# Kernel optimization log

Hardware: AMD Instinct MI355X
Metric: run time of the kernel (lower is better)

Reference implementation:

```python
import jax, jax.numpy as jnp
import numpy as np

N_NODES = 20000
N_EDGES = 320000
N_GRAPHS = 200
MAX_NODES = 100


def gcn_conv(x, W, b, src, dst, n_nodes):
    # PyG GCNConv: linear transform, add self-loops, symmetric normalization
    h = x @ W                                   # [N, out]
    loop = jnp.arange(n_nodes)
    s = jnp.concatenate([src, loop])
    d = jnp.concatenate([dst, loop])
    deg = jax.ops.segment_sum(jnp.ones_like(s, dtype=h.dtype), d, num_segments=n_nodes)
    dinv = jax.lax.rsqrt(jnp.maximum(deg, 1.0))  # deg >= 1 due to self-loops
    norm = dinv[s] * dinv[d]                     # [E+N]
    msg = h[s] * norm[:, None]                   # gather + scale
    return jax.ops.segment_sum(msg, d, num_segments=n_nodes) + b


def setup_inputs() -> dict:
    key = jax.random.key(0)
    ks = jax.random.split(key, 16)
    IN, H, L = 128, 256, 64
    P = MAX_NODES * (MAX_NODES - 1) // 2
    inp = {
        "x": jax.random.normal(ks[0], (N_NODES, IN), jnp.float32),
        "edge_index": jax.random.randint(ks[1], (2, N_EDGES), 0, N_NODES),
        "batch": jnp.sort(jax.random.randint(ks[2], (N_NODES,), 0, N_GRAPHS)),
        "eps": jax.random.normal(ks[3], (N_GRAPHS, L), jnp.float32),
        "W1": jax.random.normal(ks[4], (IN, H), jnp.float32) * (1.0 / np.sqrt(IN)),
        "b1": jnp.zeros((H,), jnp.float32),
        "W2": jax.random.normal(ks[5], (H, H), jnp.float32) * (1.0 / np.sqrt(H)),
        "b2": jnp.zeros((H,), jnp.float32),
        "Wmu": jax.random.normal(ks[6], (H, L), jnp.float32) * (1.0 / np.sqrt(H)),
        "bmu": jnp.zeros((L,), jnp.float32),
        "Wlv": jax.random.normal(ks[7], (H, L), jnp.float32) * (1.0 / np.sqrt(H)),
        "blv": jnp.zeros((L,), jnp.float32),
        "D1": jax.random.normal(ks[8], (L, H), jnp.float32) * (1.0 / np.sqrt(L)),
        "db1": jnp.zeros((H,), jnp.float32),
        "D2": jax.random.normal(ks[9], (H, H), jnp.float32) * (1.0 / np.sqrt(H)),
        "db2": jnp.zeros((H,), jnp.float32),
        "D3": jax.random.normal(ks[10], (H, P), jnp.float32) * (1.0 / np.sqrt(H)),
        "db3": jnp.zeros((P,), jnp.float32),
    }
    return inp


def reference(x, edge_index, batch, eps, W1, b1, W2, b2, Wmu, bmu, Wlv, blv,
              D1, db1, D2, db2, D3, db3):
    src, dst = edge_index[0], edge_index[1]
    # encoder
    h = jax.nn.relu(gcn_conv(x, W1, b1, src, dst, N_NODES))
    h = jax.nn.relu(gcn_conv(h, W2, b2, src, dst, N_NODES))
    # global mean pool
    sums = jax.ops.segment_sum(h, batch, num_segments=N_GRAPHS)
    cnt = jax.ops.segment_sum(jnp.ones((N_NODES,), h.dtype), batch, num_segments=N_GRAPHS)
    hg = sums / jnp.maximum(cnt, 1.0)[:, None]   # [B, H]
    mu = hg @ Wmu + bmu
    logvar = hg @ Wlv + blv
    # reparameterise
    z = mu + eps * jnp.exp(0.5 * logvar)
    # decoder MLP
    d = jax.nn.relu(z @ D1 + db1)
    d = jax.nn.relu(d @ D2 + db2)
    probs = jax.nn.sigmoid(d @ D3 + db3)         # [B, MAX_NODES*(MAX_NODES-1)//2]
    iu, ju = jnp.triu_indices(MAX_NODES, k=1)
    B = z.shape[0]
    adj = jnp.zeros((B, MAX_NODES, MAX_NODES), probs.dtype)
    adj = adj.at[:, iu, ju].set(probs)
    adj = adj + jnp.swapaxes(adj, 1, 2)
    return adj, mu, logvar
```

## Files before the change

### kernel.cpp

```cpp
#include <hip/hip_runtime.h>
#include <math.h>

#define N_NODES  20000
#define N_EDGES  320000
#define N_GRAPHS 200
#define MAXN     100
#define F_IN     128
#define F_H      256
#define F_L      64
#define P_PAIRS  4950
#define P_PAD    4992
#define ADJ_SIZE (N_GRAPHS * MAXN * MAXN)
#define MU_OFF   ADJ_SIZE
#define LV_OFF   (ADJ_SIZE + N_GRAPHS * F_L)

#define ELL_W    64
#define EF_NB    ((N_EDGES + 255) / 256)

static inline int ceil_div(int a, int b) { return (a + b - 1) / b; }

typedef __attribute__((ext_vector_type(8))) short bf16x8;
typedef __attribute__((ext_vector_type(4))) float f32x4;

static __device__ inline unsigned short f2bf(float f) {
    union { float f; unsigned u; } v; v.f = f;
    unsigned r = (v.u + 0x7FFFu + ((v.u >> 16) & 1u)) >> 16;
    return (unsigned short)r;
}
static __device__ inline float bf2f(unsigned short s) {
    union { unsigned u; float f; } v; v.u = (unsigned)s << 16; return v.f;
}
static __device__ inline float4 ubf4(ushort4 u) {
    float4 f;
    f.x = bf2f(u.x); f.y = bf2f(u.y); f.z = bf2f(u.z); f.w = bf2f(u.w);
    return f;
}
static __device__ inline float rdeg(int d) { return rsqrtf((float)d + 1.0f); }

#define PP_S1  32768
#define PP_S2  98304
#define PP_END 1376256
#define PP_NB  (PP_END / 256)
#define CV_END 640000
#define CV_NB  (CV_END / 256)
__global__ __launch_bounds__(256) void k_prep(
        const int* __restrict__ src, const int* __restrict__ dst,
        int* __restrict__ fill, int* __restrict__ ell,
        const float* __restrict__ W1, const float* __restrict__ W2,
        const float* __restrict__ D3,
        unsigned short* __restrict__ W1p, unsigned short* __restrict__ W2p,
        unsigned short* __restrict__ D3p,
        const float* __restrict__ x, unsigned short* __restrict__ xs) {
    if (blockIdx.x < EF_NB) {
        int e = blockIdx.x * 256 + threadIdx.x;
        if (e < N_EDGES) {
            int d = dst[e];
            int pos = atomicAdd(fill + d, 1);
            if (pos < ELL_W) ell[d * ELL_W + pos] = src[e];
        }
        return;
    }
    if (blockIdx.x < EF_NB + PP_NB) {
        int pid = (blockIdx.x - EF_NB) * 256 + threadIdx.x;
        const float* W; unsigned short* Bp; int N, NP, t;
        if (pid < PP_S1)      { t = pid;          W = W1; Bp = W1p; N = 256;     NP = 256; }
        else if (pid < PP_S2) { t = pid - PP_S1;  W = W2; Bp = W2p; N = 256;     NP = 256; }
        else                  { t = pid - PP_S2;  W = D3; Bp = D3p; N = P_PAIRS; NP = P_PAD; }
        int j    = t & 7;
        int lane = (t >> 3) & 63;
        int tile = t >> 9;
        int NT = NP >> 4;
        int nt = tile % NT;
        int kt = tile / NT;
        int k = kt * 32 + (lane >> 4) * 8 + j;
        int n = nt * 16 + (lane & 15);
        Bp[t] = (n < N) ? f2bf(W[(size_t)k * N + n]) : (unsigned short)0;
        return;
    }
    int tid = (blockIdx.x - EF_NB - PP_NB) * 256 + threadIdx.x;
    if (tid >= CV_END) return;
    float4 val = ((const float4*)x)[tid];
    ushort4 o;
    o.x = f2bf(val.x); o.y = f2bf(val.y);
    o.z = f2bf(val.z); o.w = f2bf(val.w);
    ((ushort4*)xs)[tid] = o;
}

__global__ __launch_bounds__(512) void k_layer1(const unsigned short* __restrict__ xs,
                                                const int* __restrict__ fill,
                                                const int* __restrict__ ell,
                                                const unsigned short* __restrict__ W1p,
                                                const float* __restrict__ bias,
                                                unsigned short* __restrict__ h1s, int M) {
    __shared__ unsigned short At[32 * 128];
    char* Ab = (char*)At;
    const int tid  = threadIdx.x;
    const int lane = tid & 63;
    const int w    = tid >> 6;

    for (int s = 0; s < 4; ++s) {
        int slot = w * 4 + s;
        int v = blockIdx.x * 32 + slot;
        ushort2 ob; ob.x = 0; ob.y = 0;
        if (v < M) {
            int dg  = fill[v];
            int beg = v * ELL_W;
            int end = beg + min(dg, ELL_W);
            float dv = rdeg(dg);
            float2 a0 = make_float2(0.f, 0.f), a1 = make_float2(0.f, 0.f);
            int i = beg;
            for (; i + 8 <= end; i += 8) {
                int s0 = ell[i + 0], s1 = ell[i + 1], s2 = ell[i + 2], s3 = ell[i + 3];
                int s4 = ell[i + 4], s5 = ell[i + 5], s6 = ell[i + 6], s7 = ell[i + 7];
                float r0 = rdeg(fill[s0]), r1 = rdeg(fill[s1]);
                float r2 = rdeg(fill[s2]), r3 = rdeg(fill[s3]);
                float r4 = rdeg(fill[s4]), r5 = rdeg(fill[s5]);
                float r6 = rdeg(fill[s6]), r7 = rdeg(fill[s7]);
                ushort2 u0 = ((const ushort2*)(xs + (size_t)s0 * F_IN))[lane];
                ushort2 u1 = ((const ushort2*)(xs + (size_t)s1 * F_IN))[lane];
                ushort2 u2 = ((const ushort2*)(xs + (size_t)s2 * F_IN))[lane];
                ushort2 u3 = ((const ushort2*)(xs + (size_t)s3 * F_IN))[lane];
                ushort2 u4 = ((const ushort2*)(xs + (size_t)s4 * F_IN))[lane];
                ushort2 u5 = ((const ushort2*)(xs + (size_t)s5 * F_IN))[lane];
                ushort2 u6 = ((const ushort2*)(xs + (size_t)s6 * F_IN))[lane];
                ushort2 u7 = ((const ushort2*)(xs + (size_t)s7 * F_IN))[lane];
                a0.x += r0 * bf2f(u0.x) + r2 * bf2f(u2.x) + r4 * bf2f(u4.x) + r6 * bf2f(u6.x);
                a0.y += r0 * bf2f(u0.y) + r2 * bf2f(u2.y) + r4 * bf2f(u4.y) + r6 * bf2f(u6.y);
                a1.x += r1 * bf2f(u1.x) + r3 * bf2f(u3.x) + r5 * bf2f(u5.x) + r7 * bf2f(u7.x);
                a1.y += r1 * bf2f(u1.y) + r3 * bf2f(u3.y) + r5 * bf2f(u5.y) + r7 * bf2f(u7.y);
            }
            for (; i + 4 <= end; i += 4) {
                int s0 = ell[i + 0], s1 = ell[i + 1], s2 = ell[i + 2], s3 = ell[i + 3];
                float r0 = rdeg(fill[s0]), r1 = rdeg(fill[s1]);
                float r2 = rdeg(fill[s2]), r3 = rdeg(fill[s3]);
                ushort2 u0 = ((const ushort2*)(xs + (size_t)s0 * F_IN))[lane];
                ushort2 u1 = ((const ushort2*)(xs + (size_t)s1 * F_IN))[lane];
                ushort2 u2 = ((const ushort2*)(xs + (size_t)s2 * F_IN))[lane];
                ushort2 u3 = ((const ushort2*)(xs + (size_t)s3 * F_IN))[lane];
                a0.x += r0 * bf2f(u0.x) + r2 * bf2f(u2.x);
                a0.y += r0 * bf2f(u0.y) + r2 * bf2f(u2.y);
                a1.x += r1 * bf2f(u1.x) + r3 * bf2f(u3.x);
                a1.y += r1 * bf2f(u1.y) + r3 * bf2f(u3.y);
            }
            for (; i < end; ++i) {
                int sv = ell[i];
                float rr = rdeg(fill[sv]);
                ushort2 u = ((const ushort2*)(xs + (size_t)sv * F_IN))[lane];
                a0.x += rr * bf2f(u.x); a0.y += rr * bf2f(u.y);
            }
            ushort2 uv = ((const ushort2*)(xs + (size_t)v * F_IN))[lane];
            ob.x = f2bf(dv * (a0.x + a1.x + dv * bf2f(uv.x)));
            ob.y = f2bf(dv * (a0.y + a1.y + dv * bf2f(uv.y)));
        }
        int byteoff = (slot * 256 + lane * 4) ^ ((slot & 7) << 4);
        *(ushort2*)(Ab + byteoff) = ob;
    }
    __syncthreads();

    const int rowhalf = w >> 2;
    const int colgrp  = w & 3;
    const int quad = lane >> 4;
    const int l15  = lane & 15;
    const int ar = rowhalf * 16 + l15;

    f32x4 acc[4];
    #pragma unroll
    for (int nt = 0; nt < 4; ++nt) acc[nt] = (f32x4){0.f, 0.f, 0.f, 0.f};

    #pragma unroll
    for (int kt = 0; kt < 4; ++kt) {
        int c = kt * 64 + quad * 16;
        bf16x8 a0 = *(const bf16x8*)(Ab + ((ar * 256 + c) ^ ((ar & 7) << 4)));
        #pragma unroll
        for (int nt = 0; nt < 4; ++nt) {
            bf16x8 b = *(const bf16x8*)(W1p + (((size_t)kt * 16 + colgrp * 4 + nt) * 64 + lane) * 8);
            acc[nt] = __builtin_amdgcn_mfma_f32_16x16x32_bf16(a0, b, acc[nt], 0, 0, 0);
        }
    }

    #pragma unroll
    for (int r = 0; r < 4; ++r) {
        int gm = blockIdx.x * 32 + rowhalf * 16 + quad * 4 + r;
        if (gm >= M) continue;
        float dv = rdeg(fill[gm]);
        #pragma unroll
        for (int nt = 0; nt < 4; ++nt) {
            int gn = colgrp * 64 + nt * 16 + l15;
            float s = acc[nt][r] + bias[gn];
            h1s[(size_t)gm * F_H + gn] = f2bf(fmaxf(s, 0.0f) * dv);
        }
    }
}

__global__ __launch_bounds__(256) void k_gemm_pool(const unsigned short* __restrict__ A,
                                                   const unsigned short* __restrict__ Bp,
                                                   const float* __restrict__ bias,
                                                   const int* __restrict__ batch,
                                                   float* __restrict__ hg, int M) {
    constexpr int KT = F_H / 32;
    const int NT   = F_H >> 4;
    const int lane = threadIdx.x & 63;
    const int wave = threadIdx.x >> 6;
    const int bm   = blockIdx.y * 64 + wave * 16;
    const int ng0  = blockIdx.x * 4;
    const int quad = lane >> 4;
    const int l15  = lane & 15;

    __shared__ float sm[64][68];
    __shared__ int gb[64];
    if (threadIdx.x < 64) {
        int gm = blockIdx.y * 64 + threadIdx.x;
        gb[threadIdx.x] = (gm < M) ? batch[gm] : -1;
    }

    int m0 = bm + l15;
    int m0c = min(m0, M - 1);

    f32x4 acc[4];
    #pragma unroll
    for (int nt = 0; nt < 4; ++nt) acc[nt] = (f32x4){0.f, 0.f, 0.f, 0.f};

    #pragma unroll
    for (int kt = 0; kt < KT; ++kt) {
        bf16x8 a0 = *(const bf16x8*)(A + (size_t)m0c * F_H + kt * 32 + quad * 8);
        #pragma unroll
        for (int nt = 0; nt < 4; ++nt) {
            bf16x8 b = *(const bf16x8*)(Bp + (((size_t)kt * NT + ng0 + nt) * 64 + lane) * 8);
            acc[nt] = __builtin_amdgcn_mfma_f32_16x16x32_bf16(a0, b, acc[nt], 0, 0, 0);
        }
    }

    #pragma unroll
    for (int r = 0; r < 4; ++r) {
        int wrow = wave * 16 + quad * 4 + r;
        #pragma unroll
        for (int nt = 0; nt < 4; ++nt) {
            int gn = ((ng0 + nt) << 4) + l15;
            sm[wrow][nt * 16 + l15] = fmaxf(acc[nt][r] + bias[gn], 0.0f);
        }
    }
    __syncthreads();

    int c  = threadIdx.x & 63;
    int r0 = (threadIdx.x >> 6) * 16;
    int gcol = blockIdx.x * 64 + c;
    float s = 0.0f;
    int cur = gb[r0];
    #pragma unroll 4
    for (int r = 0; r < 16; ++r) {
        int g = gb[r0 + r];
        if (g != cur) {
            if (cur >= 0) atomicAdd(hg + (size_t)cur * F_H + gcol, s);
            s = 0.0f; cur = g;
        }
        s += sm[r0 + r][c];
    }
    if (cur >= 0) atomicAdd(hg + (size_t)cur * F_H + gcol, s);
}

__global__ __launch_bounds__(512) void k_gather2(const unsigned short* __restrict__ Hs,
                                                 const int* __restrict__ fill,
                                                 const int* __restrict__ ell,
                                                 unsigned short* __restrict__ outp) {
    __shared__ float4 part[4][64];
    int w = threadIdx.x >> 6;
    int nl = w >> 1;
    int half = w & 1;
    int v = blockIdx.x * 4 + nl;
    int lane = threadIdx.x & 63;
    int dg  = fill[v];
    int beg = v * ELL_W;
    int end = beg + min(dg, ELL_W);
    int mid = beg + ((end - beg) >> 1);
    int lo = half ? mid : beg;
    int hi = half ? end : mid;
    float4 a0 = make_float4(0.f, 0.f, 0.f, 0.f);
    float4 a1 = make_float4(0.f, 0.f, 0.f, 0.f);
    int i = lo;
    for (; i + 8 <= hi; i += 8) {
        int s0 = ell[i + 0], s1 = ell[i + 1], s2 = ell[i + 2], s3 = ell[i + 3];
        int s4 = ell[i + 4], s5 = ell[i + 5], s6 = ell[i + 6], s7 = ell[i + 7];
        float4 h0 = ubf4(((const ushort4*)(Hs + (size_t)s0 * F_H))[lane]);
        float4 h1 = ubf4(((const ushort4*)(Hs + (size_t)s1 * F_H))[lane]);
        float4 h2 = ubf4(((const ushort4*)(Hs + (size_t)s2 * F_H))[lane]);
        float4 h3 = ubf4(((const ushort4*)(Hs + (size_t)s3 * F_H))[lane]);
        float4 h4 = ubf4(((const ushort4*)(Hs + (size_t)s4 * F_H))[lane]);
        float4 h5 = ubf4(((const ushort4*)(Hs + (size_t)s5 * F_H))[lane]);
        float4 h6 = ubf4(((const ushort4*)(Hs + (size_t)s6 * F_H))[lane]);
        float4 h7 = ubf4(((const ushort4*)(Hs + (size_t)s7 * F_H))[lane]);
        a0.x += h0.x + h2.x + h4.x + h6.x; a0.y += h0.y + h2.y + h4.y + h6.y;
        a0.z += h0.z + h2.z + h4.z + h6.z; a0.w += h0.w + h2.w + h4.w + h6.w;
        a1.x += h1.x + h3.x + h5.x + h7.x; a1.y += h1.y + h3.y + h5.y + h7.y;
        a1.z += h1.z + h3.z + h5.z + h7.z; a1.w += h1.w + h3.w + h5.w + h7.w;
    }
    for (; i + 4 <= hi; i += 4) {
        int s0 = ell[i + 0], s1 = ell[i + 1], s2 = ell[i + 2], s3 = ell[i + 3];
        float4 h0 = ubf4(((const ushort4*)(Hs + (size_t)s0 * F_H))[lane]);
        float4 h1 = ubf4(((const ushort4*)(Hs + (size_t)s1 * F_H))[lane]);
        float4 h2 = ubf4(((const ushort4*)(Hs + (size_t)s2 * F_H))[lane]);
        float4 h3 = ubf4(((const ushort4*)(Hs + (size_t)s3 * F_H))[lane]);
        a0.x += h0.x + h2.x; a0.y += h0.y + h2.y; a0.z += h0.z + h2.z; a0.w += h0.w + h2.w;
        a1.x += h1.x + h3.x; a1.y += h1.y + h3.y; a1.z += h1.z + h3.z; a1.w += h1.w + h3.w;
    }
    for (; i < hi; ++i) {
        int s = ell[i];
        float4 h = ubf4(((const ushort4*)(Hs + (size_t)s * F_H))[lane]);
        a0.x += h.x; a0.y += h.y; a0.z += h.z; a0.w += h.w;
    }
    if (half) part[nl][lane] = make_float4(a0.x + a1.x, a0.y + a1.y,
                                           a0.z + a1.z, a0.w + a1.w);
    __syncthreads();
    if (!half) {
        float4 p = part[nl][lane];
        float dv = rdeg(dg);
        float4 hv = ubf4(((const ushort4*)(Hs + (size_t)v * F_H))[lane]);
        float ox = dv * (a0.x + a1.x + p.x + hv.x);
        float oy = dv * (a0.y + a1.y + p.y + hv.y);
        float oz = dv * (a0.z + a1.z + p.z + hv.z);
        float ow = dv * (a0.w + a1.w + p.w + hv.w);
        ushort4 ob;
        ob.x = f2bf(ox); ob.y = f2bf(oy); ob.z = f2bf(oz); ob.w = f2bf(ow);
        ((ushort4*)outp)[(size_t)v * 64 + lane] = ob;
    }
}

__global__ __launch_bounds__(256) void k_head_dec(const float* __restrict__ hg,
                                                  const int* __restrict__ batch,
                                                  const float* __restrict__ Wmu,
                                                  const float* __restrict__ bmu,
                                                  const float* __restrict__ Wlv,
                                                  const float* __restrict__ blv,
                                                  const float* __restrict__ eps,
                                                  const float* __restrict__ D1,
                                                  const float* __restrict__ db1,
                                                  const float* __restrict__ D2,
                                                  const float* __restrict__ db2,
                                                  float* __restrict__ out,
                                                  unsigned short* __restrict__ d2b) {
    int g = blockIdx.x;
    int tid = threadIdx.x;
    __shared__ float hgs[F_H];
    __shared__ float pp[256];
    __shared__ float mulv[128];
    __shared__ float zs[F_L];
    __shared__ float d1s[F_H];
    __shared__ float sInv;
    if (tid == 0) {
        int lo = 0, hi = N_NODES;
        while (lo < hi) { int mid = (lo + hi) >> 1; if (batch[mid] < g) lo = mid + 1; else hi = mid; }
        int beg = lo;
        hi = N_NODES;
        while (lo < hi) { int mid = (lo + hi) >> 1; if (batch[mid] < g + 1) lo = mid + 1; else hi = mid; }
        sInv = 1.0f / fmaxf((float)(lo - beg), 1.0f);
    }
    __syncthreads();
    hgs[tid] = hg[(size_t)g * F_H + tid] * sInv;
    __syncthreads();
    {
        int o    = tid & 127;
        int half = tid >> 7;
        int l = o & 63;
        const float* W = (o < 64) ? Wmu : Wlv;
        float s = 0.0f;
        int k0 = half * 128;
        #pragma unroll 8
        for (int k = k0; k < k0 + 128; ++k) s += hgs[k] * W[(size_t)k * F_L + l];
        pp[tid] = s;
    }
    __syncthreads();
    if (tid < 128) {
        int l = tid & 63;
        float s = pp[tid] + pp[tid + 128] + ((tid < 64) ? bmu[l] : blv[l]);
        out[((tid < 64) ? MU_OFF : LV_OFF) + g * F_L + l] = s;
        mulv[tid] = s;
    }
    __syncthreads();
    if (tid < 64)
        zs[tid] = mulv[tid] + eps[g * F_L + tid] * expf(0.5f * mulv[64 + tid]);
    __syncthreads();
    {
        float s = db1[tid];
        #pragma unroll 8
        for (int k = 0; k < F_L; ++k) s += zs[k] * D1[(size_t)k * F_H + tid];
        d1s[tid] = fmaxf(s, 0.0f);
    }
    __syncthreads();
    {
        float s = db2[tid];
        #pragma unroll 8
        for (int k = 0; k < F_H; ++k) s += d1s[k] * D2[(size_t)k * F_H + tid];
        d2b[(size_t)g * F_H + tid] = f2bf(fmaxf(s, 0.0f));
    }
}

__global__ __launch_bounds__(256) void k_gemm3(const unsigned short* __restrict__ A,
                                               const unsigned short* __restrict__ Bp,
                                               float* __restrict__ Y,
                                               const float* __restrict__ bias,
                                               int M, int N, int NP) {
    constexpr int KT = F_H / 32;
    const int NT   = NP >> 4;
    const int lane = threadIdx.x & 63;
    const int wave = threadIdx.x >> 6;
    const int bm   = blockIdx.y * 32;
    const int ng   = blockIdx.x * 4 + wave;
    const int quad = lane >> 4;
    const int l15  = lane & 15;

    int m0 = bm + l15;
    int m1 = m0 + 16;
    int m0c = min(m0, M - 1), m1c = min(m1, M - 1);

    f32x4 acc[2];
    acc[0] = (f32x4){0.f, 0.f, 0.f, 0.f};
    acc[1] = (f32x4){0.f, 0.f, 0.f, 0.f};

    #pragma unroll
    for (int kt = 0; kt < KT; ++kt) {
        bf16x8 a0 = *(const bf16x8*)(A + (size_t)m0c * F_H + kt * 32 + quad * 8);
        bf16x8 a1 = *(const bf16x8*)(A + (size_t)m1c * F_H + kt * 32 + quad * 8);
        bf16x8 b = *(const bf16x8*)(Bp + (((size_t)kt * NT + ng) * 64 + lane) * 8);
        acc[0] = __builtin_amdgcn_mfma_f32_16x16x32_bf16(a0, b, acc[0], 0, 0, 0);
        acc[1] = __builtin_amdgcn_mfma_f32_16x16x32_bf16(a1, b, acc[1], 0, 0, 0);
    }

    #pragma unroll
    for (int i = 0; i < 2; ++i) {
        #pragma unroll
        for (int r = 0; r < 4; ++r) {
            int gm = bm + i * 16 + quad * 4 + r;
            if (gm >= M) continue;
            int gn = (ng << 4) + l15;
            if (gn >= N) continue;
            float s = acc[i][r] + bias[gn];
            Y[(size_t)gm * N + gn] = 1.0f / (1.0f + expf(-s));
        }
    }
}

__global__ __launch_bounds__(256) void k_adj(const float* __restrict__ probs,
                                             float* __restrict__ adj) {
    int i = blockIdx.x * blockDim.x + threadIdx.x;
    if (i >= N_GRAPHS * MAXN * (MAXN / 4)) return;
    int b4 = (i % (MAXN / 4)) * 4;
    int a  = (i / (MAXN / 4)) % MAXN;
    int g  = i / (MAXN * (MAXN / 4));
    const float* pg = probs + (size_t)g * P_PAIRS;
    float4 o;
    float* op = (float*)&o;
    #pragma unroll
    for (int c = 0; c < 4; ++c) {
        int b = b4 + c;
        float v = 0.0f;
        if (a != b) {
            int lo = min(a, b), hi = max(a, b);
            int p = lo * (MAXN - 1) - (lo * (lo - 1)) / 2 + (hi - lo - 1);
            v = pg[p];
        }
        op[c] = v;
    }
    ((float4*)adj)[i] = o;
}

extern "C" void kernel_launch(void* const* d_in, const int* in_sizes, int n_in,
                              void* d_out, int out_size, void* d_ws, size_t ws_size,
                              hipStream_t stream) {
    const float* x    = (const float*)d_in[0];
    const int*   eidx = (const int*)d_in[1];
    const int*   batch= (const int*)d_in[2];
    const float* eps  = (const float*)d_in[3];
    const float* W1   = (const float*)d_in[4];
    const float* b1   = (const float*)d_in[5];
    const float* W2   = (const float*)d_in[6];
    const float* b2   = (const float*)d_in[7];
    const float* Wmu  = (const float*)d_in[8];
    const float* bmu  = (const float*)d_in[9];
    const float* Wlv  = (const float*)d_in[10];
    const float* blv  = (const float*)d_in[11];
    const float* D1   = (const float*)d_in[12];
    const float* db1  = (const float*)d_in[13];
    const float* D2   = (const float*)d_in[14];
    const float* db2  = (const float*)d_in[15];
    const float* D3   = (const float*)d_in[16];
    const float* db3  = (const float*)d_in[17];

    const int* src = eidx;
    const int* dst = eidx + N_EDGES;
    float* out = (float*)d_out;

    char* wsb = (char*)d_ws;
    size_t o = 0;
    auto carve = [&](size_t bytes) { void* p = wsb + o; o += (bytes + 255) & ~255ull; return p; };
    int*   fill   = (int*)  carve(N_NODES * sizeof(int));
    float* hg     = (float*)carve((size_t)N_GRAPHS * F_H * sizeof(float));
    int*   ell    = (int*)  carve((size_t)N_NODES * ELL_W * sizeof(int));
    unsigned short* xs  = (unsigned short*)carve((size_t)N_NODES * F_IN * sizeof(short));
    unsigned short* W1p = (unsigned short*)carve((size_t)F_IN * F_H * sizeof(short));
    unsigned short* W2p = (unsigned short*)carve((size_t)F_H * F_H * sizeof(short));
    unsigned short* D3p = (unsigned short*)carve((size_t)F_H * P_PAD * sizeof(short));
    unsigned short* h1s = (unsigned short*)carve((size_t)N_NODES * F_H * sizeof(short));
    unsigned short* g2  = (unsigned short*)carve((size_t)N_NODES * F_H * sizeof(short));
    unsigned short* d2b = (unsigned short*)carve((size_t)N_GRAPHS * F_H * sizeof(short));
    float* probs  = (float*)carve((size_t)N_GRAPHS * P_PAIRS * sizeof(float));

    hipMemsetAsync(fill, 0, 284928, stream);
    k_prep<<<EF_NB + PP_NB + CV_NB, 256, 0, stream>>>(src, dst, fill, ell,
                                                      W1, W2, D3, W1p, W2p, D3p,
                                                      x, xs);

    k_layer1<<<ceil_div(N_NODES, 32), 512, 0, stream>>>(xs, fill, ell,
                                                        W1p, b1, h1s, N_NODES);

    k_gather2<<<N_NODES / 4, 512, 0, stream>>>(h1s, fill, ell, g2);
    {
        dim3 grid(F_H / 64, ceil_div(N_NODES, 64));
        k_gemm_pool<<<grid, 256, 0, stream>>>(g2, W2p, b2, batch, hg, N_NODES);
    }

    k_head_dec<<<N_GRAPHS, 256, 0, stream>>>(hg, batch, Wmu, bmu, Wlv, blv, eps,
                                             D1, db1, D2, db2, out, d2b);

    {
        dim3 grid(P_PAD / 64, ceil_div(N_GRAPHS, 32));
        k_gemm3<<<grid, 256, 0, stream>>>(d2b, D3p, probs, db3,
                                          N_GRAPHS, P_PAIRS, P_PAD);
    }

    k_adj<<<ceil_div(N_GRAPHS * MAXN * (MAXN / 4), 256), 256, 0, stream>>>(probs, out);
}
```

Before: 219.4 us.

## Fuse layer-2 neighbor gather with GEMM and mean-pool into one kernel

Replaces the separate gather2 kernel and gemm_pool kernel with a single k_layer2 kernel. Each block first gathers 32 aggregated node rows into swizzled shared memory, then runs the MFMA GEMM against W2 over all 256 output columns and finishes with the ReLU and atomic pool into hg. This removes the g2 intermediate write and read through global memory and one launch. In exchange each wave gathers four nodes sequentially instead of splitting one node's edges across two waves, which lowers gather parallelism per node, and the block now uses a large shared buffer that may limit occupancy.

Measured after the change: 212.8 us. -3.0%, faster.

```diff
diff --git a/kernel.cpp b/kernel.cpp
--- a/kernel.cpp
+++ b/kernel.cpp
@@ -192,136 +192,126 @@
     }
 }
 
-__global__ __launch_bounds__(256) void k_gemm_pool(const unsigned short* __restrict__ A,
-                                                   const unsigned short* __restrict__ Bp,
-                                                   const float* __restrict__ bias,
-                                                   const int* __restrict__ batch,
-                                                   float* __restrict__ hg, int M) {
-    constexpr int KT = F_H / 32;
-    const int NT   = F_H >> 4;
-    const int lane = threadIdx.x & 63;
-    const int wave = threadIdx.x >> 6;
-    const int bm   = blockIdx.y * 64 + wave * 16;
-    const int ng0  = blockIdx.x * 4;
+__global__ __launch_bounds__(512) void k_layer2(const unsigned short* __restrict__ h1s,
+                                                const int* __restrict__ fill,
+                                                const int* __restrict__ ell,
+                                                const unsigned short* __restrict__ W2p,
+                                                const float* __restrict__ bias,
+                                                const int* __restrict__ batch,
+                                                float* __restrict__ hg, int M) {
+    __shared__ __align__(16) char smem[32 * 260 * 4];
+    __shared__ int gb[32];
+    char* Ab = smem;
+    const int tid  = threadIdx.x;
+    const int lane = tid & 63;
+    const int w    = tid >> 6;
+
+    if (tid < 32) {
+        int gm = blockIdx.x * 32 + tid;
+        gb[tid] = (gm < M) ? batch[gm] : -1;
+    }
+
+    for (int s = 0; s < 4; ++s) {
+        int slot = w * 4 + s;
+        int v = blockIdx.x * 32 + slot;
+        ushort4 ob; ob.x = ob.y = ob.z = ob.w = 0;
+        if (v < M) {
+            int dg  = fill[v];
+            int beg = v * ELL_W;
+            int end = beg + min(dg, ELL_W);
+            float4 a0 = make_float4(0.f, 0.f, 0.f, 0.f);
+            float4 a1 = make_float4(0.f, 0.f, 0.f, 0.f);
+            int i = beg;
+            for (; i + 8 <= end; i += 8) {
+                int s0 = ell[i + 0], s1 = ell[i + 1], s2 = ell[i + 2], s3 = ell[i + 3];
+                int s4 = ell[i + 4], s5 = ell[i + 5], s6 = ell[i + 6], s7 = ell[i + 7];
+                float4 h0 = ubf4(((const ushort4*)(h1s + (size_t)s0 * F_H))[lane]);
+                float4 h1 = ubf4(((const ushort4*)(h1s + (size_t)s1 * F_H))[lane]);
+                float4 h2 = ubf4(((const ushort4*)(h1s + (size_t)s2 * F_H))[lane]);
+                float4 h3 = ubf4(((const ushort4*)(h1s + (size_t)s3 * F_H))[lane]);
+                float4 h4 = ubf4(((const ushort4*)(h1s + (size_t)s4 * F_H))[lane]);
+                float4 h5 = ubf4(((const ushort4*)(h1s + (size_t)s5 * F_H))[lane]);
+                float4 h6 = ubf4(((const ushort4*)(h1s + (size_t)s6 * F_H))[lane]);
+                float4 h7 = ubf4(((const ushort4*)(h1s + (size_t)s7 * F_H))[lane]);
+                a0.x += h0.x + h2.x + h4.x + h6.x; a0.y += h0.y + h2.y + h4.y + h6.y;
+                a0.z += h0.z + h2.z + h4.z + h6.z; a0.w += h0.w + h2.w + h4.w + h6.w;
+                a1.x += h1.x + h3.x + h5.x + h7.x; a1.y += h1.y + h3.y + h5.y + h7.y;
+                a1.z += h1.z + h3.z + h5.z + h7.z; a1.w += h1.w + h3.w + h5.w + h7.w;
+            }
+            for (; i + 4 <= end; i += 4) {
+                int s0 = ell[i + 0], s1 = ell[i + 1], s2 = ell[i + 2], s3 = ell[i + 3];
+                float4 h0 = ubf4(((const ushort4*)(h1s + (size_t)s0 * F_H))[lane]);
+                float4 h1 = ubf4(((const ushort4*)(h1s + (size_t)s1 * F_H))[lane]);
+                float4 h2 = ubf4(((const ushort4*)(h1s + (size_t)s2 * F_H))[lane]);
+                float4 h3 = ubf4(((const ushort4*)(h1s + (size_t)s3 * F_H))[lane]);
+                a0.x += h0.x + h2.x; a0.y += h0.y + h2.y; a0.z += h0.z + h2.z; a0.w += h0.w + h2.w;
+                a1.x += h1.x + h3.x; a1.y += h1.y + h3.y; a1.z += h1.z + h3.z; a1.w += h1.w + h3.w;
+            }
+            for (; i < end; ++i) {
+                int sv = ell[i];
+                float4 h = ubf4(((const ushort4*)(h1s + (size_t)sv * F_H))[lane]);
+                a0.x += h.x; a0.y += h.y; a0.z += h.z; a0.w += h.w;
+            }
+            float dv = rdeg(dg);
+            float4 hv = ubf4(((const ushort4*)(h1s + (size_t)v * F_H))[lane]);
+            ob.x = f2bf(dv * (a0.x + a1.x + hv.x));
+            ob.y = f2bf(dv * (a0.y + a1.y + hv.y));
+            ob.z = f2bf(dv * (a0.z + a1.z + hv.z));
+            ob.w = f2bf(dv * (a0.w + a1.w + hv.w));
+        }
+        int byteoff = (slot * 512 + lane * 8) ^ ((slot & 7) << 4);
+        *(ushort4*)(Ab + byteoff) = ob;
+    }
+    __syncthreads();
+
+    const int rowhalf = w >> 2;
+    const int colgrp  = w & 3;
     const int quad = lane >> 4;
     const int l15  = lane & 15;
-
-    __shared__ float sm[64][68];
-    __shared__ int gb[64];
-    if (threadIdx.x < 64) {
-        int gm = blockIdx.y * 64 + threadIdx.x;
-        gb[threadIdx.x] = (gm < M) ? batch[gm] : -1;
-    }
-
-    int m0 = bm + l15;
-    int m0c = min(m0, M - 1);
+    const int ar = rowhalf * 16 + l15;
 
     f32x4 acc[4];
     #pragma unroll
     for (int nt = 0; nt < 4; ++nt) acc[nt] = (f32x4){0.f, 0.f, 0.f, 0.f};
 
     #pragma unroll
-    for (int kt = 0; kt < KT; ++kt) {
-        bf16x8 a0 = *(const bf16x8*)(A + (size_t)m0c * F_H + kt * 32 + quad * 8);
+    for (int kt = 0; kt < 8; ++kt) {
+        int cb = kt * 64 + quad * 16;
+        bf16x8 a0 = *(const bf16x8*)(Ab + ((ar * 512 + cb) ^ ((ar & 7) << 4)));
         #pragma unroll
         for (int nt = 0; nt < 4; ++nt) {
-            bf16x8 b = *(const bf16x8*)(Bp + (((size_t)kt * NT + ng0 + nt) * 64 + lane) * 8);
+            bf16x8 b = *(const bf16x8*)(W2p + (((size_t)kt * 16 + colgrp * 4 + nt) * 64 + lane) * 8);
             acc[nt] = __builtin_amdgcn_mfma_f32_16x16x32_bf16(a0, b, acc[nt], 0, 0, 0);
         }
     }
-
+    __syncthreads();
+
+    float* sm = (float*)smem;
     #pragma unroll
     for (int r = 0; r < 4; ++r) {
-        int wrow = wave * 16 + quad * 4 + r;
+        int wrow = rowhalf * 16 + quad * 4 + r;
         #pragma unroll
         for (int nt = 0; nt < 4; ++nt) {
-            int gn = ((ng0 + nt) << 4) + l15;
-            sm[wrow][nt * 16 + l15] = fmaxf(acc[nt][r] + bias[gn], 0.0f);
-        }
-    }
-    __syncthreads();
-
-    int c  = threadIdx.x & 63;
-    int r0 = (threadIdx.x >> 6) * 16;
-    int gcol = blockIdx.x * 64 + c;
+            int cl = colgrp * 64 + nt * 16 + l15;
+            sm[wrow * 260 + cl] = fmaxf(acc[nt][r] + bias[cl], 0.0f);
+        }
+    }
+    __syncthreads();
+
+    int c  = tid & 255;
+    int r0 = (tid >> 8) * 16;
     float s = 0.0f;
     int cur = gb[r0];
     #pragma unroll 4
     for (int r = 0; r < 16; ++r) {
         int g = gb[r0 + r];
         if (g != cur) {
-            if (cur >= 0) atomicAdd(hg + (size_t)cur * F_H + gcol, s);
+            if (cur >= 0) atomicAdd(hg + (size_t)cur * F_H + c, s);
             s = 0.0f; cur = g;
         }
-        s += sm[r0 + r][c];
-    }
-    if (cur >= 0) atomicAdd(hg + (size_t)cur * F_H + gcol, s);
-}
-
-__global__ __launch_bounds__(512) void k_gather2(const unsigned short* __restrict__ Hs,
-                                                 const int* __restrict__ fill,
-                                                 const int* __restrict__ ell,
-                                                 unsigned short* __restrict__ outp) {
-    __shared__ float4 part[4][64];
-    int w = threadIdx.x >> 6;
-    int nl = w >> 1;
-    int half = w & 1;
-    int v = blockIdx.x * 4 + nl;
-    int lane = threadIdx.x & 63;
-    int dg  = fill[v];
-    int beg = v * ELL_W;
-    int end = beg + min(dg, ELL_W);
-    int mid = beg + ((end - beg) >> 1);
-    int lo = half ? mid : beg;
-    int hi = half ? end : mid;
-    float4 a0 = make_float4(0.f, 0.f, 0.f, 0.f);
-    float4 a1 = make_float4(0.f, 0.f, 0.f, 0.f);
-    int i = lo;
-    for (; i + 8 <= hi; i += 8) {
-        int s0 = ell[i + 0], s1 = ell[i + 1], s2 = ell[i + 2], s3 = ell[i + 3];
-        int s4 = ell[i + 4], s5 = ell[i + 5], s6 = ell[i + 6], s7 = ell[i + 7];
-        float4 h0 = ubf4(((const ushort4*)(Hs + (size_t)s0 * F_H))[lane]);
-        float4 h1 = ubf4(((const ushort4*)(Hs + (size_t)s1 * F_H))[lane]);
-        float4 h2 = ubf4(((const ushort4*)(Hs + (size_t)s2 * F_H))[lane]);
-        float4 h3 = ubf4(((const ushort4*)(Hs + (size_t)s3 * F_H))[lane]);
-        float4 h4 = ubf4(((const ushort4*)(Hs + (size_t)s4 * F_H))[lane]);
-        float4 h5 = ubf4(((const ushort4*)(Hs + (size_t)s5 * F_H))[lane]);
-        float4 h6 = ubf4(((const ushort4*)(Hs + (size_t)s6 * F_H))[lane]);
-        float4 h7 = ubf4(((const ushort4*)(Hs + (size_t)s7 * F_H))[lane]);
-        a0.x += h0.x + h2.x + h4.x + h6.x; a0.y += h0.y + h2.y + h4.y + h6.y;
-        a0.z += h0.z + h2.z + h4.z + h6.z; a0.w += h0.w + h2.w + h4.w + h6.w;
-        a1.x += h1.x + h3.x + h5.x + h7.x; a1.y += h1.y + h3.y + h5.y + h7.y;
-        a1.z += h1.z + h3.z + h5.z + h7.z; a1.w += h1.w + h3.w + h5.w + h7.w;
-    }
-    for (; i + 4 <= hi; i += 4) {
-        int s0 = ell[i + 0], s1 = ell[i + 1], s2 = ell[i + 2], s3 = ell[i + 3];
-        float4 h0 = ubf4(((const ushort4*)(Hs + (size_t)s0 * F_H))[lane]);
-        float4 h1 = ubf4(((const ushort4*)(Hs + (size_t)s1 * F_H))[lane]);
-        float4 h2 = ubf4(((const ushort4*)(Hs + (size_t)s2 * F_H))[lane]);
-        float4 h3 = ubf4(((const ushort4*)(Hs + (size_t)s3 * F_H))[lane]);
-        a0.x += h0.x + h2.x; a0.y += h0.y + h2.y; a0.z += h0.z + h2.z; a0.w += h0.w + h2.w;
-        a1.x += h1.x + h3.x; a1.y += h1.y + h3.y; a1.z += h1.z + h3.z; a1.w += h1.w + h3.w;
-    }
-    for (; i < hi; ++i) {
-        int s = ell[i];
-        float4 h = ubf4(((const ushort4*)(Hs + (size_t)s * F_H))[lane]);
-        a0.x += h.x; a0.y += h.y; a0.z += h.z; a0.w += h.w;
-    }
-    if (half) part[nl][lane] = make_float4(a0.x + a1.x, a0.y + a1.y,
-                                           a0.z + a1.z, a0.w + a1.w);
-    __syncthreads();
-    if (!half) {
-        float4 p = part[nl][lane];
-        float dv = rdeg(dg);
-        float4 hv = ubf4(((const ushort4*)(Hs + (size_t)v * F_H))[lane]);
-        float ox = dv * (a0.x + a1.x + p.x + hv.x);
-        float oy = dv * (a0.y + a1.y + p.y + hv.y);
-        float oz = dv * (a0.z + a1.z + p.z + hv.z);
-        float ow = dv * (a0.w + a1.w + p.w + hv.w);
-        ushort4 ob;
-        ob.x = f2bf(ox); ob.y = f2bf(oy); ob.z = f2bf(oz); ob.w = f2bf(ow);
-        ((ushort4*)outp)[(size_t)v * 64 + lane] = ob;
-    }
+        s += sm[(r0 + r) * 260 + c];
+    }
+    if (cur >= 0) atomicAdd(hg + (size_t)cur * F_H + c, s);
 }
 
 __global__ __launch_bounds__(256) void k_head_dec(const float* __restrict__ hg,
@@ -499,7 +489,6 @@
     unsigned short* W2p = (unsigned short*)carve((size_t)F_H * F_H * sizeof(short));
     unsigned short* D3p = (unsigned short*)carve((size_t)F_H * P_PAD * sizeof(short));
     unsigned short* h1s = (unsigned short*)carve((size_t)N_NODES * F_H * sizeof(short));
-    unsigned short* g2  = (unsigned short*)carve((size_t)N_NODES * F_H * sizeof(short));
     unsigned short* d2b = (unsigned short*)carve((size_t)N_GRAPHS * F_H * sizeof(short));
     float* probs  = (float*)carve((size_t)N_GRAPHS * P_PAIRS * sizeof(float));
 
@@ -511,11 +500,8 @@
     k_layer1<<<ceil_div(N_NODES, 32), 512, 0, stream>>>(xs, fill, ell,
                                                         W1p, b1, h1s, N_NODES);
 
-    k_gather2<<<N_NODES / 4, 512, 0, stream>>>(h1s, fill, ell, g2);
-    {
-        dim3 grid(F_H / 64, ceil_div(N_NODES, 64));
-        k_gemm_pool<<<grid, 256, 0, stream>>>(g2, W2p, b2, batch, hg, N_NODES);
-    }
+    k_layer2<<<ceil_div(N_NODES, 32), 512, 0, stream>>>(h1s, fill, ell,
+                                                        W2p, b2, batch, hg, N_NODES);
 
     k_head_dec<<<N_GRAPHS, 256, 0, stream>>>(hg, batch, Wmu, bmu, Wlv, blv, eps,
                                              D1, db1, D2, db2, out, d2b);
```
